# Kernel tuning notes

Hardware: AMD Instinct MI355X
Metric: run time of the kernel (lower is better)

Reference implementation:

```python
import jax, jax.numpy as jnp
import numpy as np

B, S, D, H = 2, 2048, 512, 8
DK = D // H


def setup_inputs() -> dict:
    key = jax.random.key(0)
    ks = jax.random.split(key, 6)
    q = jax.random.normal(ks[0], (B, S, D), dtype=jnp.float32)
    k = jax.random.normal(ks[1], (B, S, D), dtype=jnp.float32)
    v = jax.random.normal(ks[2], (B, S, D), dtype=jnp.float32)
    mask = jax.random.randint(ks[3], (1, 1, S, S), 0, 2, dtype=jnp.int32)
    # nn.Linear weights [out, in]; scaled like torch default init
    Wq = jax.random.normal(ks[4], (D, D), dtype=jnp.float32) / np.sqrt(D)
    Wo = jax.random.normal(ks[5], (D, D), dtype=jnp.float32) / np.sqrt(D)
    return {"q": q, "k": k, "v": v, "mask": mask, "Wq": Wq, "Wo": Wo}


def _split_heads(x):
    # [B,S,D] -> [B,H,S,DK]
    return x.reshape(B, S, H, DK).transpose(0, 2, 1, 3)


def reference(q, k, v, mask, Wq, Wo):
    # NOTE: original module applies Wq to q, k AND v (faithful to source bug)
    query = _split_heads(q @ Wq.T)
    key_ = _split_heads(k @ Wq.T)
    value = _split_heads(v @ Wq.T)
    scores = jnp.einsum("bhqd,bhkd->bhqk", query, key_) / np.sqrt(DK).astype(np.float32)
    # original uses masked_fill_(mask==0, 1e-09) BEFORE softmax (not -inf)
    scores = jnp.where(mask == 0, jnp.float32(1e-9), scores)
    attn = jax.nn.softmax(scores, axis=-1)  # dropout p=0.0 -> identity
    x = jnp.einsum("bhqk,bhkd->bhqd", attn, value)
    x = x.transpose(0, 2, 1, 3).reshape(B, S, D)
    return x @ Wo.T
```

## Files before the change

kernel.cpp:

```cpp
#include <hip/hip_runtime.h>
#include <hip/hip_bf16.h>
#include <stdint.h>

#define S_LEN 2048
#define D_MOD 512
#define N_H   8
#define D_K   64

typedef short v8s __attribute__((ext_vector_type(8)));
typedef short v4s __attribute__((ext_vector_type(4)));
typedef float v4f __attribute__((ext_vector_type(4)));

__device__ __forceinline__ short f2bf(float f) {
  union { float f; unsigned u; } a; a.f = f;
  unsigned u = a.u;
  u += 0x7fffu + ((u >> 16) & 1u);
  return (short)(u >> 16);
}
__device__ __forceinline__ short f2bfh(float f) {
  union { float f; unsigned u; } a; a.f = f;
  return (short)((a.u + 0x8000u) >> 16);
}
__device__ __forceinline__ float bf2f(short s) {
  union { unsigned u; float f; } x;
  x.u = ((unsigned)(unsigned short)s) << 16;
  return x.f;
}
__device__ __forceinline__ unsigned pk2(float a, float b) {
  unsigned r;
  asm("v_cvt_pk_bf16_f32 %0, %1, %2" : "=v"(r) : "v"(a), "v"(b));
  return r;
}

__device__ __forceinline__ v4f mfma16(v8s a, v8s b, v4f c) {
  return __builtin_amdgcn_mfma_f32_16x16x32_bf16(a, b, c, 0, 0, 0);
}
__device__ __forceinline__ v4f mfma16x16(v4s a, v4s b, v4f c) {
  return __builtin_amdgcn_mfma_f32_16x16x16bf16_1k(a, b, c, 0, 0, 0);
}

__global__ __launch_bounds__(256) void proj_kernel(
    const float* __restrict__ q, const float* __restrict__ k,
    const float* __restrict__ v, const float* __restrict__ Wq,
    const float* __restrict__ Wo, const int* __restrict__ mask,
    short* __restrict__ QP, short* __restrict__ KP, short* __restrict__ VT,
    short* __restrict__ Wob, unsigned long long* __restrict__ mp)
{
  const int tid = threadIdx.x;
  if (blockIdx.z == 1) {
    int bid = blockIdx.x * 8 + blockIdx.y;
    if (bid < 256) {
      int id = bid * 256 + tid;
      const int4* m4 = (const int4*)(mask + (size_t)id * 64);
      unsigned long long w = 0ull;
#pragma unroll
      for (int j = 0; j < 16; j++) {
        int4 mv = m4[j];
        w |= (unsigned long long)(mv.x != 0) << (j * 4 + 0);
        w |= (unsigned long long)(mv.y != 0) << (j * 4 + 1);
        w |= (unsigned long long)(mv.z != 0) << (j * 4 + 2);
        w |= (unsigned long long)(mv.w != 0) << (j * 4 + 3);
      }
      mp[id] = w;
    } else {
      unsigned off = (bid - 256) * 256 + tid;
      float4 x = ((const float4*)Wo)[off];
      v4s p; p.x = f2bf(x.x); p.y = f2bf(x.y); p.z = f2bf(x.z); p.w = f2bf(x.w);
      ((v4s*)Wob)[off] = p;
    }
    return;
  }
  const int m0 = blockIdx.x * 64, n0 = blockIdx.y * 64;
  const int wave = tid >> 6, lane = tid & 63;
  const int quad = lane >> 4, l15 = lane & 15;
  const int wm = wave >> 1, wn = wave & 1;
  const float* Az[3] = {q, k, v};
  __shared__ short As[3][64][72];
  __shared__ short Bs[64][72];
  v4f acc[3][2][2];
#pragma unroll
  for (int z = 0; z < 3; z++)
#pragma unroll
    for (int i = 0; i < 2; i++)
#pragma unroll
      for (int j = 0; j < 2; j++) acc[z][i][j] = (v4f){0.f, 0.f, 0.f, 0.f};

  float4 a4[3][4], b4[4];
#pragma unroll
  for (int i = 0; i < 4; i++) {
    int fi = tid + i * 256, r = fi >> 4, c = (fi & 15) << 2;
#pragma unroll
    for (int z = 0; z < 3; z++)
      a4[z][i] = *(const float4*)&Az[z][(m0 + r) * 512 + c];
    b4[i] = *(const float4*)&Wq[(n0 + r) * 512 + c];
  }

  for (int kk = 0; kk < 512; kk += 64) {
    __syncthreads();
#pragma unroll
    for (int i = 0; i < 4; i++) {
      int fi = tid + i * 256, r = fi >> 4, c = (fi & 15) << 2;
#pragma unroll
      for (int z = 0; z < 3; z++) {
        union { unsigned u[2]; v4s s; } ap;
        ap.u[0] = pk2(a4[z][i].x, a4[z][i].y);
        ap.u[1] = pk2(a4[z][i].z, a4[z][i].w);
        *(v4s*)&As[z][r][c] = ap.s;
      }
      union { unsigned u[2]; v4s s; } bp;
      bp.u[0] = pk2(b4[i].x, b4[i].y);
      bp.u[1] = pk2(b4[i].z, b4[i].w);
      *(v4s*)&Bs[r][c] = bp.s;
    }
    __syncthreads();
    if (kk + 64 < 512) {
#pragma unroll
      for (int i = 0; i < 4; i++) {
        int fi = tid + i * 256, r = fi >> 4, c = (fi & 15) << 2;
#pragma unroll
        for (int z = 0; z < 3; z++)
          a4[z][i] = *(const float4*)&Az[z][(m0 + r) * 512 + kk + 64 + c];
        b4[i] = *(const float4*)&Wq[(n0 + r) * 512 + kk + 64 + c];
      }
    }
#pragma unroll
    for (int ns = 0; ns < 2; ns++)
#pragma unroll
      for (int ks = 0; ks < 2; ks++) {
        union { v8s v; v4s h2[2]; } bb;
        bb.h2[0] = *(const v4s*)&Bs[wn * 32 + ns * 16 + l15][ks * 32 + quad * 8];
        bb.h2[1] = *(const v4s*)&Bs[wn * 32 + ns * 16 + l15][ks * 32 + quad * 8 + 4];
#pragma unroll
        for (int ms = 0; ms < 2; ms++)
#pragma unroll
          for (int z = 0; z < 3; z++) {
            union { v8s v; v4s h2[2]; } a;
            a.h2[0] = *(const v4s*)&As[z][wm * 32 + ms * 16 + l15][ks * 32 + quad * 8];
            a.h2[1] = *(const v4s*)&As[z][wm * 32 + ms * 16 + l15][ks * 32 + quad * 8 + 4];
            acc[z][ms][ns] = mfma16(a.v, bb.v, acc[z][ms][ns]);
          }
      }
  }
#pragma unroll
  for (int z = 0; z < 3; z++)
#pragma unroll
    for (int ms = 0; ms < 2; ms++)
#pragma unroll
      for (int ns = 0; ns < 2; ns++) {
        int mb = m0 + wm * 32 + ms * 16 + quad * 4;
        int n  = n0 + wn * 32 + ns * 16 + l15;
        int bI = mb >> 11, s = mb & 2047, hh = n >> 6, dk = n & 63;
        if (z == 2) {
          v4s pv;
          pv.x = f2bf(acc[z][ms][ns][0]); pv.y = f2bf(acc[z][ms][ns][1]);
          pv.z = f2bf(acc[z][ms][ns][2]); pv.w = f2bf(acc[z][ms][ns][3]);
          *(v4s*)&VT[((bI * N_H + hh) * D_K + dk) * S_LEN + s] = pv;
        } else {
          short* dst = (z == 0) ? QP : KP;
#pragma unroll
          for (int r = 0; r < 4; r++)
            dst[((bI * N_H + hh) * S_LEN + (s + r)) * D_K + dk] = f2bf(acc[z][ms][ns][r]);
        }
      }
}

__global__ __launch_bounds__(512, 4) void attn_kernel(
    const short* __restrict__ QP, const short* __restrict__ KP,
    const short* __restrict__ VT, const unsigned long long* __restrict__ MP,
    short* __restrict__ X)
{
  const int qt = blockIdx.x;
  const int h = blockIdx.y, b = blockIdx.z;
  const int tid = threadIdx.x;
  const int wave = tid >> 6, lane = tid & 63;
  const int quad = lane >> 4, l15 = lane & 15;
  const int qw = wave & 3, kg = wave >> 2;
  const short* Qh = QP + ((b * N_H + h) * S_LEN) * D_K;
  const short* Kh = KP + ((b * N_H + h) * S_LEN) * D_K;
  const short* Vh = VT + ((b * N_H + h) * D_K) * S_LEN;

  __shared__ short SMEM[2][2][2][64][64];

  const int qrow = qt * 64 + qw * 16;
  const int srow = tid >> 3;
  const int sc8  = (tid & 7) * 8;
  const int scw  = sc8 ^ ((srow & 7) << 3);
  const int swz  = (l15 & 7) << 3;

  v8s aQ[2];
#pragma unroll
  for (int ks = 0; ks < 2; ks++)
    aQ[ks] = *(const v8s*)&Qh[(qrow + l15) * D_K + ks * 32 + quad * 8];

  const float C1 = 0.18033688011112042f;
  const float C2 = -11.541560327111707f;
  const v4s ONES4 = {16256, 16256, 16256, 16256};
  v4f accX[4], accL = (v4f){0.f, 0.f, 0.f, 0.f};
#pragma unroll
  for (int u = 0; u < 4; u++) accX[u] = (v4f){0.f, 0.f, 0.f, 0.f};

  v8s kr0 = *(const v8s*)&Kh[srow * D_K + sc8];
  v8s vr0 = *(const v8s*)&Vh[srow * S_LEN + sc8];
  v8s kr1 = *(const v8s*)&Kh[(64 + srow) * D_K + sc8];
  v8s vr1 = *(const v8s*)&Vh[srow * S_LEN + 64 + sc8];
  *(v8s*)&SMEM[0][0][0][srow][scw] = kr0;
  *(v8s*)&SMEM[0][0][1][srow][scw] = vr0;
  *(v8s*)&SMEM[0][1][0][srow][scw] = kr1;
  *(v8s*)&SMEM[0][1][1][srow][scw] = vr1;
  unsigned long long mwc = MP[(qrow + l15) * 32 + kg];
  unsigned long long mwn = 0ull;
  __syncthreads();

  for (int it = 0; it < 16; it++) {
    const int p = it & 1;
    if (it + 1 < 16) {
      const int c0 = (it + 1) * 128, c1 = c0 + 64;
      kr0 = *(const v8s*)&Kh[(c0 + srow) * D_K + sc8];
      vr0 = *(const v8s*)&Vh[srow * S_LEN + c0 + sc8];
      kr1 = *(const v8s*)&Kh[(c1 + srow) * D_K + sc8];
      vr1 = *(const v8s*)&Vh[srow * S_LEN + c1 + sc8];
      mwn = MP[(qrow + l15) * 32 + 2 * (it + 1) + kg];
    }

    v4s pa[4];
#pragma unroll
    for (int tp = 0; tp < 4; tp++) {
      v8s bK0 = *(const v8s*)&SMEM[p][kg][0][tp * 16 + l15][(quad * 8) ^ swz];
      v8s bK1 = *(const v8s*)&SMEM[p][kg][0][tp * 16 + l15][(32 + quad * 8) ^ swz];
      v4f s = mfma16(bK0, aQ[0], (v4f){0.f, 0.f, 0.f, 0.f});
      s = mfma16(bK1, aQ[1], s);
      unsigned mb = (unsigned)(mwc >> (tp * 16 + quad * 4));
      v4s pk;
#pragma unroll
      for (int r = 0; r < 4; r++) {
        float se = ((mb >> r) & 1u) ? s[r] : 0.0f;
        float pr = __builtin_amdgcn_exp2f(fmaf(se, C1, C2));
        pk[r] = f2bfh(pr);
      }
      pa[tp] = pk;
    }

#pragma unroll
    for (int u = 0; u < 4; u++) {
      const short* vb_ = &SMEM[p][kg][1][u * 16 + l15][0];
#pragma unroll
      for (int tp = 0; tp < 4; tp++) {
        v4s bV = *(const v4s*)&vb_[(tp * 16 + quad * 4) ^ swz];
        accX[u] = mfma16x16(pa[tp], bV, accX[u]);
      }
    }
#pragma unroll
    for (int tp = 0; tp < 4; tp++)
      accL = mfma16x16(pa[tp], ONES4, accL);

    if (it + 1 < 16) {
      *(v8s*)&SMEM[p ^ 1][0][0][srow][scw] = kr0;
      *(v8s*)&SMEM[p ^ 1][0][1][srow][scw] = vr0;
      *(v8s*)&SMEM[p ^ 1][1][0][srow][scw] = kr1;
      *(v8s*)&SMEM[p ^ 1][1][1][srow][scw] = vr1;
    }
    __syncthreads();
    mwc = mwn;
  }

  float* ex = (float*)&SMEM[0][0][0][0][0];
  const int xi = (qw * 64 + lane) * 21;
  if (kg == 1) {
#pragma unroll
    for (int u = 0; u < 4; u++)
#pragma unroll
      for (int r = 0; r < 4; r++) ex[xi + u * 4 + r] = accX[u][r];
#pragma unroll
    for (int r = 0; r < 4; r++) ex[xi + 16 + r] = accL[r];
  }
  __syncthreads();
  if (kg == 0) {
#pragma unroll
    for (int u = 0; u < 4; u++)
#pragma unroll
      for (int r = 0; r < 4; r++) accX[u][r] += ex[xi + u * 4 + r];
#pragma unroll
    for (int r = 0; r < 4; r++) accL[r] += ex[xi + 16 + r];
    v4f linv;
#pragma unroll
    for (int r = 0; r < 4; r++) linv[r] = 1.0f / accL[r];
#pragma unroll
    for (int u = 0; u < 4; u++)
#pragma unroll
      for (int r = 0; r < 4; r++) {
        int srw = qrow + quad * 4 + r;
        X[(b * S_LEN + srw) * D_MOD + h * D_K + u * 16 + l15] =
            f2bf(accX[u][r] * linv[r]);
      }
  }
}

__global__ __launch_bounds__(256) void outproj_kernel(
    const short* __restrict__ X, const short* __restrict__ Wob,
    float* __restrict__ out)
{
  const int m0 = blockIdx.x * 64, n0 = blockIdx.y * 64;
  const int tid = threadIdx.x;
  const int wave = tid >> 6, lane = tid & 63;
  const int quad = lane >> 4, l15 = lane & 15;
  const int wm = wave >> 1, wn = wave & 1;
  __shared__ short As[64][72];
  __shared__ short Bs[64][72];

  v4f acc[2][2];
#pragma unroll
  for (int i = 0; i < 2; i++)
#pragma unroll
    for (int j = 0; j < 2; j++) acc[i][j] = (v4f){0.f, 0.f, 0.f, 0.f};

  v8s a8[2], b8[2];
#pragma unroll
  for (int i = 0; i < 2; i++) {
    int fi = tid + i * 256, r = fi >> 3, c = (fi & 7) << 3;
    a8[i] = *(const v8s*)&X[(m0 + r) * 512 + c];
    b8[i] = *(const v8s*)&Wob[(n0 + r) * 512 + c];
  }

  for (int kk = 0; kk < 512; kk += 64) {
    __syncthreads();
#pragma unroll
    for (int i = 0; i < 2; i++) {
      int fi = tid + i * 256, r = fi >> 3, c = (fi & 7) << 3;
      *(v8s*)&As[r][c] = a8[i];
      *(v8s*)&Bs[r][c] = b8[i];
    }
    __syncthreads();
    if (kk + 64 < 512) {
#pragma unroll
      for (int i = 0; i < 2; i++) {
        int fi = tid + i * 256, r = fi >> 3, c = (fi & 7) << 3;
        a8[i] = *(const v8s*)&X[(m0 + r) * 512 + kk + 64 + c];
        b8[i] = *(const v8s*)&Wob[(n0 + r) * 512 + kk + 64 + c];
      }
    }
#pragma unroll
    for (int ms = 0; ms < 2; ms++)
#pragma unroll
      for (int ns = 0; ns < 2; ns++)
#pragma unroll
        for (int ks = 0; ks < 2; ks++) {
          union { v8s v; v4s h2[2]; } a, bb;
          a.h2[0]  = *(const v4s*)&As[wm * 32 + ms * 16 + l15][ks * 32 + quad * 8];
          a.h2[1]  = *(const v4s*)&As[wm * 32 + ms * 16 + l15][ks * 32 + quad * 8 + 4];
          bb.h2[0] = *(const v4s*)&Bs[wn * 32 + ns * 16 + l15][ks * 32 + quad * 8];
          bb.h2[1] = *(const v4s*)&Bs[wn * 32 + ns * 16 + l15][ks * 32 + quad * 8 + 4];
          acc[ms][ns] = mfma16(a.v, bb.v, acc[ms][ns]);
        }
  }
#pragma unroll
  for (int ms = 0; ms < 2; ms++)
#pragma unroll
    for (int ns = 0; ns < 2; ns++) {
      int n = n0 + wn * 32 + ns * 16 + l15;
#pragma unroll
      for (int r = 0; r < 4; r++) {
        int m = m0 + wm * 32 + ms * 16 + quad * 4 + r;
        out[m * 512 + n] = acc[ms][ns][r];
      }
    }
}

extern "C" void kernel_launch(void* const* d_in, const int* in_sizes, int n_in,
                              void* d_out, int out_size, void* d_ws, size_t ws_size,
                              hipStream_t stream) {
  const float* q  = (const float*)d_in[0];
  const float* k  = (const float*)d_in[1];
  const float* v  = (const float*)d_in[2];
  const int* mask = (const int*)d_in[3];
  const float* Wq = (const float*)d_in[4];
  const float* Wo = (const float*)d_in[5];
  float* out = (float*)d_out;
  char* ws = (char*)d_ws;
  short* QP = (short*)(ws);
  short* KP = (short*)(ws + (4u << 20));
  short* VT = (short*)(ws + (8u << 20));
  unsigned long long* MP = (unsigned long long*)(ws + (16u << 20));
  short* Wob = (short*)(ws + (16u << 20) + (512u << 10));
  short* X  = (short*)(ws + (17u << 20));

  proj_kernel<<<dim3(64, 8, 2), 256, 0, stream>>>(q, k, v, Wq, Wo, mask,
                                                  QP, KP, VT, Wob, MP);
  attn_kernel<<<dim3(32, N_H, 2), 512, 0, stream>>>(QP, KP, VT, MP, X);
  outproj_kernel<<<dim3(64, 8, 1), 256, 0, stream>>>(X, Wob, out);
}
```

Before: 140.4 us.

## Halve attention block to 4 waves, each computing two 16-row query subtiles

The attention kernel now runs 256 threads (4 waves) per block instead of 512. Each wave processes 32 query rows as two 16-row subtiles, so every K and V fragment read from shared memory feeds twice as many MFMAs. Each thread loads two 8-element chunks per K/V tile to keep the cooperative load complete. This cuts LDS traffic per FLOP and raises instruction-level parallelism, but it doubles accumulator registers per wave and leaves fewer waves per block to hide latency.

```diff
diff --git a/kernel.cpp b/kernel.cpp
--- a/kernel.cpp
+++ b/kernel.cpp
@@ -164,7 +164,7 @@
       }
 }
 
-__global__ __launch_bounds__(512, 4) void attn_kernel(
+__global__ __launch_bounds__(256, 2) void attn_kernel(
     const short* __restrict__ QP, const short* __restrict__ KP,
     const short* __restrict__ VT, const unsigned long long* __restrict__ MP,
     short* __restrict__ X)
@@ -174,70 +174,95 @@
   const int tid = threadIdx.x;
   const int wave = tid >> 6, lane = tid & 63;
   const int quad = lane >> 4, l15 = lane & 15;
-  const int qw = wave & 3, kg = wave >> 2;
+  const int qw = wave & 1, kg = wave >> 1;
   const short* Qh = QP + ((b * N_H + h) * S_LEN) * D_K;
   const short* Kh = KP + ((b * N_H + h) * S_LEN) * D_K;
   const short* Vh = VT + ((b * N_H + h) * D_K) * S_LEN;
 
   __shared__ short SMEM[2][2][2][64][64];
 
-  const int qrow = qt * 64 + qw * 16;
-  const int srow = tid >> 3;
-  const int sc8  = (tid & 7) * 8;
-  const int scw  = sc8 ^ ((srow & 7) << 3);
+  const int qrowb = qt * 64 + qw * 32;
+  const int srow = tid >> 2;
+  const int sc0  = (tid & 3) * 16;
+  const int sw   = (srow & 7) << 3;
+  const int scw0 = sc0 ^ sw, scw1 = (sc0 + 8) ^ sw;
   const int swz  = (l15 & 7) << 3;
 
-  v8s aQ[2];
-#pragma unroll
-  for (int ks = 0; ks < 2; ks++)
-    aQ[ks] = *(const v8s*)&Qh[(qrow + l15) * D_K + ks * 32 + quad * 8];
+  v8s aQ[2][2];
+#pragma unroll
+  for (int qs = 0; qs < 2; qs++)
+#pragma unroll
+    for (int ks = 0; ks < 2; ks++)
+      aQ[qs][ks] = *(const v8s*)&Qh[(qrowb + qs * 16 + l15) * D_K + ks * 32 + quad * 8];
 
   const float C1 = 0.18033688011112042f;
   const float C2 = -11.541560327111707f;
   const v4s ONES4 = {16256, 16256, 16256, 16256};
-  v4f accX[4], accL = (v4f){0.f, 0.f, 0.f, 0.f};
-#pragma unroll
-  for (int u = 0; u < 4; u++) accX[u] = (v4f){0.f, 0.f, 0.f, 0.f};
-
-  v8s kr0 = *(const v8s*)&Kh[srow * D_K + sc8];
-  v8s vr0 = *(const v8s*)&Vh[srow * S_LEN + sc8];
-  v8s kr1 = *(const v8s*)&Kh[(64 + srow) * D_K + sc8];
-  v8s vr1 = *(const v8s*)&Vh[srow * S_LEN + 64 + sc8];
-  *(v8s*)&SMEM[0][0][0][srow][scw] = kr0;
-  *(v8s*)&SMEM[0][0][1][srow][scw] = vr0;
-  *(v8s*)&SMEM[0][1][0][srow][scw] = kr1;
-  *(v8s*)&SMEM[0][1][1][srow][scw] = vr1;
-  unsigned long long mwc = MP[(qrow + l15) * 32 + kg];
-  unsigned long long mwn = 0ull;
+  v4f accX[2][4], accL[2];
+#pragma unroll
+  for (int qs = 0; qs < 2; qs++) {
+    accL[qs] = (v4f){0.f, 0.f, 0.f, 0.f};
+#pragma unroll
+    for (int u = 0; u < 4; u++) accX[qs][u] = (v4f){0.f, 0.f, 0.f, 0.f};
+  }
+
+  v8s kr[2][2], vr[2][2];
+#pragma unroll
+  for (int par = 0; par < 2; par++) {
+    const int ck = par * 64;
+    kr[par][0] = *(const v8s*)&Kh[(ck + srow) * D_K + sc0];
+    kr[par][1] = *(const v8s*)&Kh[(ck + srow) * D_K + sc0 + 8];
+    vr[par][0] = *(const v8s*)&Vh[srow * S_LEN + ck + sc0];
+    vr[par][1] = *(const v8s*)&Vh[srow * S_LEN + ck + sc0 + 8];
+  }
+#pragma unroll
+  for (int par = 0; par < 2; par++) {
+    *(v8s*)&SMEM[0][par][0][srow][scw0] = kr[par][0];
+    *(v8s*)&SMEM[0][par][0][srow][scw1] = kr[par][1];
+    *(v8s*)&SMEM[0][par][1][srow][scw0] = vr[par][0];
+    *(v8s*)&SMEM[0][par][1][srow][scw1] = vr[par][1];
+  }
+  unsigned long long mwc[2], mwn[2] = {0ull, 0ull};
+#pragma unroll
+  for (int qs = 0; qs < 2; qs++)
+    mwc[qs] = MP[(qrowb + qs * 16 + l15) * 32 + kg];
   __syncthreads();
 
   for (int it = 0; it < 16; it++) {
     const int p = it & 1;
     if (it + 1 < 16) {
-      const int c0 = (it + 1) * 128, c1 = c0 + 64;
-      kr0 = *(const v8s*)&Kh[(c0 + srow) * D_K + sc8];
-      vr0 = *(const v8s*)&Vh[srow * S_LEN + c0 + sc8];
-      kr1 = *(const v8s*)&Kh[(c1 + srow) * D_K + sc8];
-      vr1 = *(const v8s*)&Vh[srow * S_LEN + c1 + sc8];
-      mwn = MP[(qrow + l15) * 32 + 2 * (it + 1) + kg];
-    }
-
-    v4s pa[4];
+#pragma unroll
+      for (int par = 0; par < 2; par++) {
+        const int ck = (it + 1) * 128 + par * 64;
+        kr[par][0] = *(const v8s*)&Kh[(ck + srow) * D_K + sc0];
+        kr[par][1] = *(const v8s*)&Kh[(ck + srow) * D_K + sc0 + 8];
+        vr[par][0] = *(const v8s*)&Vh[srow * S_LEN + ck + sc0];
+        vr[par][1] = *(const v8s*)&Vh[srow * S_LEN + ck + sc0 + 8];
+      }
+#pragma unroll
+      for (int qs = 0; qs < 2; qs++)
+        mwn[qs] = MP[(qrowb + qs * 16 + l15) * 32 + 2 * (it + 1) + kg];
+    }
+
+    v4s pa[2][4];
 #pragma unroll
     for (int tp = 0; tp < 4; tp++) {
       v8s bK0 = *(const v8s*)&SMEM[p][kg][0][tp * 16 + l15][(quad * 8) ^ swz];
       v8s bK1 = *(const v8s*)&SMEM[p][kg][0][tp * 16 + l15][(32 + quad * 8) ^ swz];
-      v4f s = mfma16(bK0, aQ[0], (v4f){0.f, 0.f, 0.f, 0.f});
-      s = mfma16(bK1, aQ[1], s);
-      unsigned mb = (unsigned)(mwc >> (tp * 16 + quad * 4));
-      v4s pk;
-#pragma unroll
-      for (int r = 0; r < 4; r++) {
-        float se = ((mb >> r) & 1u) ? s[r] : 0.0f;
-        float pr = __builtin_amdgcn_exp2f(fmaf(se, C1, C2));
-        pk[r] = f2bfh(pr);
-      }
-      pa[tp] = pk;
+#pragma unroll
+      for (int qs = 0; qs < 2; qs++) {
+        v4f s = mfma16(bK0, aQ[qs][0], (v4f){0.f, 0.f, 0.f, 0.f});
+        s = mfma16(bK1, aQ[qs][1], s);
+        unsigned mb = (unsigned)(mwc[qs] >> (tp * 16 + quad * 4));
+        v4s pk;
+#pragma unroll
+        for (int r = 0; r < 4; r++) {
+          float se = ((mb >> r) & 1u) ? s[r] : 0.0f;
+          float pr = __builtin_amdgcn_exp2f(fmaf(se, C1, C2));
+          pk[r] = f2bfh(pr);
+        }
+        pa[qs][tp] = pk;
+      }
     }
 
 #pragma unroll
@@ -246,52 +271,65 @@
 #pragma unroll
       for (int tp = 0; tp < 4; tp++) {
         v4s bV = *(const v4s*)&vb_[(tp * 16 + quad * 4) ^ swz];
-        accX[u] = mfma16x16(pa[tp], bV, accX[u]);
-      }
-    }
-#pragma unroll
-    for (int tp = 0; tp < 4; tp++)
-      accL = mfma16x16(pa[tp], ONES4, accL);
+        accX[0][u] = mfma16x16(pa[0][tp], bV, accX[0][u]);
+        accX[1][u] = mfma16x16(pa[1][tp], bV, accX[1][u]);
+      }
+    }
+#pragma unroll
+    for (int qs = 0; qs < 2; qs++)
+#pragma unroll
+      for (int tp = 0; tp < 4; tp++)
+        accL[qs] = mfma16x16(pa[qs][tp], ONES4, accL[qs]);
 
     if (it + 1 < 16) {
-      *(v8s*)&SMEM[p ^ 1][0][0][srow][scw] = kr0;
-      *(v8s*)&SMEM[p ^ 1][0][1][srow][scw] = vr0;
-      *(v8s*)&SMEM[p ^ 1][1][0][srow][scw] = kr1;
-      *(v8s*)&SMEM[p ^ 1][1][1][srow][scw] = vr1;
+#pragma unroll
+      for (int par = 0; par < 2; par++) {
+        *(v8s*)&SMEM[p ^ 1][par][0][srow][scw0] = kr[par][0];
+        *(v8s*)&SMEM[p ^ 1][par][0][srow][scw1] = kr[par][1];
+        *(v8s*)&SMEM[p ^ 1][par][1][srow][scw0] = vr[par][0];
+        *(v8s*)&SMEM[p ^ 1][par][1][srow][scw1] = vr[par][1];
+      }
     }
     __syncthreads();
-    mwc = mwn;
+    mwc[0] = mwn[0]; mwc[1] = mwn[1];
   }
 
   float* ex = (float*)&SMEM[0][0][0][0][0];
-  const int xi = (qw * 64 + lane) * 21;
   if (kg == 1) {
 #pragma unroll
-    for (int u = 0; u < 4; u++)
-#pragma unroll
-      for (int r = 0; r < 4; r++) ex[xi + u * 4 + r] = accX[u][r];
-#pragma unroll
-    for (int r = 0; r < 4; r++) ex[xi + 16 + r] = accL[r];
+    for (int qs = 0; qs < 2; qs++) {
+      int xi = ((qw * 2 + qs) * 64 + lane) * 21;
+#pragma unroll
+      for (int u = 0; u < 4; u++)
+#pragma unroll
+        for (int r = 0; r < 4; r++) ex[xi + u * 4 + r] = accX[qs][u][r];
+#pragma unroll
+      for (int r = 0; r < 4; r++) ex[xi + 16 + r] = accL[qs][r];
+    }
   }
   __syncthreads();
   if (kg == 0) {
 #pragma unroll
-    for (int u = 0; u < 4; u++)
-#pragma unroll
-      for (int r = 0; r < 4; r++) accX[u][r] += ex[xi + u * 4 + r];
-#pragma unroll
-    for (int r = 0; r < 4; r++) accL[r] += ex[xi + 16 + r];
-    v4f linv;
-#pragma unroll
-    for (int r = 0; r < 4; r++) linv[r] = 1.0f / accL[r];
-#pragma unroll
-    for (int u = 0; u < 4; u++)
-#pragma unroll
-      for (int r = 0; r < 4; r++) {
-        int srw = qrow + quad * 4 + r;
-        X[(b * S_LEN + srw) * D_MOD + h * D_K + u * 16 + l15] =
-            f2bf(accX[u][r] * linv[r]);
-      }
+    for (int qs = 0; qs < 2; qs++) {
+      int xi = ((qw * 2 + qs) * 64 + lane) * 21;
+#pragma unroll
+      for (int u = 0; u < 4; u++)
+#pragma unroll
+        for (int r = 0; r < 4; r++) accX[qs][u][r] += ex[xi + u * 4 + r];
+#pragma unroll
+      for (int r = 0; r < 4; r++) accL[qs][r] += ex[xi + 16 + r];
+      v4f linv;
+#pragma unroll
+      for (int r = 0; r < 4; r++) linv[r] = 1.0f / accL[qs][r];
+#pragma unroll
+      for (int u = 0; u < 4; u++)
+#pragma unroll
+        for (int r = 0; r < 4; r++) {
+          int srw = qrowb + qs * 16 + quad * 4 + r;
+          X[(b * S_LEN + srw) * D_MOD + h * D_K + u * 16 + l15] =
+              f2bf(accX[qs][u][r] * linv[r]);
+        }
+    }
   }
 }
 
@@ -385,6 +423,6 @@
 
   proj_kernel<<<dim3(64, 8, 2), 256, 0, stream>>>(q, k, v, Wq, Wo, mask,
                                                   QP, KP, VT, Wob, MP);
-  attn_kernel<<<dim3(32, N_H, 2), 512, 0, stream>>>(QP, KP, VT, MP, X);
+  attn_kernel<<<dim3(32, N_H, 2), 256, 0, stream>>>(QP, KP, VT, MP, X);
   outproj_kernel<<<dim3(64, 8, 1), 256, 0, stream>>>(X, Wob, out);
 }
```

After: 145.4 us. 3.6% more time.
